# Kernel optimization log

Measured on AMD Instinct MI355X. Metric: run time of the kernel, lower is better.

The kernel has to match this reference:

```python
import jax, jax.numpy as jnp
import numpy as np

H = 1024
V = 50257
S = 8192


def setup_inputs() -> dict:
    key = jax.random.key(0)
    ks = jax.random.split(key, 13)
    s = 0.02  # param init scale
    return {
        "input": jax.random.randint(ks[0], (1,), 0, V),
        "hidden": jax.random.normal(ks[1], (1, 1, H), jnp.float32),
        "encoder_outputs": jax.random.normal(ks[2], (S, H), jnp.float32),
        "embedding": jax.random.normal(ks[3], (V, H), jnp.float32) * s,
        "attn_w": jax.random.normal(ks[4], (1, 2 * H), jnp.float32) * s,
        "attn_b": jnp.zeros((1,), jnp.float32),
        "comb_w": jax.random.normal(ks[5], (H, 2 * H), jnp.float32) * s,
        "comb_b": jnp.zeros((H,), jnp.float32),
        "w_ih": jax.random.normal(ks[6], (3 * H, H), jnp.float32) * s,
        "w_hh": jax.random.normal(ks[7], (3 * H, H), jnp.float32) * s,
        "b_ih": jnp.zeros((3 * H,), jnp.float32),
        "b_hh": jnp.zeros((3 * H,), jnp.float32),
        "out_w": jax.random.normal(ks[8], (V, H), jnp.float32) * s,
        "out_b": jnp.zeros((V,), jnp.float32),
    }


def reference(input, hidden, encoder_outputs, embedding, attn_w, attn_b,
              comb_w, comb_b, w_ih, w_hh, b_ih, b_hh, out_w, out_b):
    # embedded = embedding(input).view(1,1,-1); dropout in eval mode = identity
    emb = embedding[input[0]]            # [H]
    h0 = hidden[0, 0]                    # [H]
    # Original loop computes the SAME score attn(cat(emb, hidden)) for every
    # timestep -> softmax over a constant vector (uniform weights). Compute the
    # scalar once and broadcast (same math, one GEMV instead of S launches).
    score = jnp.concatenate([emb, h0]) @ attn_w[0] + attn_b[0]   # scalar
    seq_len = encoder_outputs.shape[0]
    attn_weights = jax.nn.softmax(jnp.broadcast_to(score, (seq_len,)))  # [S]
    attn_applied = attn_weights @ encoder_outputs                # [H]
    combined = jnp.concatenate([emb, attn_applied]) @ comb_w.T + comb_b  # [H]
    x = jax.nn.relu(combined)
    # Single GRU step (torch nn.GRU gate math)
    gi = w_ih @ x + b_ih                 # [3H]
    gh = w_hh @ h0 + b_hh                # [3H]
    i_r, i_z, i_n = jnp.split(gi, 3)
    h_r, h_z, h_n = jnp.split(gh, 3)
    r = jax.nn.sigmoid(i_r + h_r)
    z = jax.nn.sigmoid(i_z + h_z)
    n = jnp.tanh(i_n + r * h_n)
    h_new = (1.0 - z) * n + z * h0       # [H]
    logits = h_new @ out_w.T + out_b     # [V]
    output = jax.nn.log_softmax(logits)[None, :]   # [1, V]
    return output, h_new[None, None, :], attn_weights[None, :]
```

## Files before the change

kernel.cpp:

```cpp
#include <hip/hip_runtime.h>
#include <math.h>

#define HN 1024
#define VN 50257
#define SN 8192

#define WS_PARTIAL 0
#define WS_AA      262144
#define WS_X       263168
#define WS_GH      264192
#define WS_CEMB    267264
#define WS_HNEW    270336
#define WS_LOGITS  271360
#define WS_EXPD    321618

__device__ __forceinline__ float wred(float v) {
#pragma unroll
  for (int m = 32; m; m >>= 1) v += __shfl_xor(v, m);
  return v;
}

__device__ __forceinline__ float dot4(float4 a, float4 b) {
  return a.x * b.x + a.y * b.y + a.z * b.z + a.w * b.w;
}

__global__ __launch_bounds__(1024) void k1_front(
    const float* __restrict__ enc, const float* __restrict__ w_hh,
    const float* __restrict__ hidden, const int* __restrict__ token,
    const float* __restrict__ embedding, const float* __restrict__ comb_w,
    const float* __restrict__ comb_b, float* __restrict__ ws,
    float* __restrict__ out_attn) {
  const int blk = blockIdx.x, t = threadIdx.x;
  if (blk < 256) {
    __shared__ float4 lds[1024];
    const int g = t >> 8, c4 = t & 255;
    const float4* e4 = (const float4*)enc + ((size_t)blk * 32 + g * 8) * 256 + c4;
    float4 acc = make_float4(0.f, 0.f, 0.f, 0.f);
#pragma unroll
    for (int r = 0; r < 8; ++r) {
      float4 v = e4[r * 256];
      acc.x += v.x; acc.y += v.y; acc.z += v.z; acc.w += v.w;
    }
    lds[t] = acc;
    __syncthreads();
    if (t < 256) {
      float4 a = lds[t], b = lds[t + 256], c = lds[t + 512], d = lds[t + 768];
      float4 s = make_float4(a.x + b.x + c.x + d.x, a.y + b.y + c.y + d.y,
                             a.z + b.z + c.z + d.z, a.w + b.w + c.w + d.w);
      ((float4*)(ws + WS_PARTIAL))[blk * 256 + t] = s;
    }
    if (t < 32) out_attn[blk * 32 + t] = 1.f / 8192.f;
  } else if (blk < 320) {
    const int wg = (blk - 256) * 16 + (t >> 6);
    const int l = t & 63;
    const float4* h4 = (const float4*)hidden;
    float4 hv0 = h4[l], hv1 = h4[64 + l], hv2 = h4[128 + l], hv3 = h4[192 + l];
#pragma unroll
    for (int k = 0; k < 3; ++k) {
      const int r = wg + k * 1024;
      const float4* m4 = (const float4*)w_hh + (size_t)r * 256;
      float acc = dot4(m4[l], hv0) + dot4(m4[64 + l], hv1) +
                  dot4(m4[128 + l], hv2) + dot4(m4[192 + l], hv3);
      acc = wred(acc);
      if (l == 0) ws[WS_GH + r] = acc;
    }
  } else {
    const int i = (blk - 320) * 16 + (t >> 6);
    const int l = t & 63;
    const int tok = token[0];
    const float4* emb4 = (const float4*)embedding + (size_t)tok * 256;
    const float4* cw4 = (const float4*)comb_w + (size_t)i * 512;
    float acc = 0.f;
#pragma unroll
    for (int k = 0; k < 4; ++k) acc += dot4(cw4[k * 64 + l], emb4[k * 64 + l]);
    acc = wred(acc);
    if (l == 0) ws[WS_CEMB + i] = acc + comb_b[i];
  }
}

__global__ void k2_reduce(float* __restrict__ ws) {
  __shared__ float lds[256];
  const int t = threadIdx.x, b = blockIdx.x;
  const int c = b * 32 + (t & 31), rg = t >> 5;
  const float* p = ws + WS_PARTIAL;
  float s = 0.f;
#pragma unroll 8
  for (int j = 0; j < 32; ++j) s += p[(rg * 32 + j) * 1024 + c];
  lds[t] = s;
  __syncthreads();
  if (t < 32) {
    float a = 0.f;
#pragma unroll
    for (int j = 0; j < 8; ++j) a += lds[j * 32 + t];
    ws[WS_AA + b * 32 + t] = a * (1.f / 8192.f);
  }
}

__global__ void k3_x(const float* __restrict__ comb_w, float* __restrict__ ws) {
  const int w = threadIdx.x >> 6, l = threadIdx.x & 63;
  const int i = blockIdx.x * 4 + w;
  const float4* aa4 = (const float4*)(ws + WS_AA);
  const float4* cw4 = (const float4*)comb_w + (size_t)i * 512 + 256;
  float acc = 0.f;
#pragma unroll
  for (int k = 0; k < 4; ++k) acc += dot4(cw4[k * 64 + l], aa4[k * 64 + l]);
  acc = wred(acc);
  if (l == 0) ws[WS_X + i] = fmaxf(ws[WS_CEMB + i] + acc, 0.f);
}

__global__ void k4_gates_h(const float* __restrict__ w_ih,
                           const float* __restrict__ b_ih, const float* __restrict__ b_hh,
                           const float* __restrict__ hidden, float* __restrict__ ws,
                           float* __restrict__ d_out) {
  const int w = threadIdx.x >> 6, l = threadIdx.x & 63;
  const int i = blockIdx.x * 4 + w;
  const float4* x4 = (const float4*)(ws + WS_X);
  float4 xv0 = x4[l], xv1 = x4[64 + l], xv2 = x4[128 + l], xv3 = x4[192 + l];
  const float4* m0 = (const float4*)w_ih + (size_t)i * 256;
  const float4* m1 = (const float4*)w_ih + (size_t)(i + 1024) * 256;
  const float4* m2 = (const float4*)w_ih + (size_t)(i + 2048) * 256;
  float a0 = dot4(m0[l], xv0) + dot4(m0[64 + l], xv1) +
             dot4(m0[128 + l], xv2) + dot4(m0[192 + l], xv3);
  float a1 = dot4(m1[l], xv0) + dot4(m1[64 + l], xv1) +
             dot4(m1[128 + l], xv2) + dot4(m1[192 + l], xv3);
  float a2 = dot4(m2[l], xv0) + dot4(m2[64 + l], xv1) +
             dot4(m2[128 + l], xv2) + dot4(m2[192 + l], xv3);
  a0 = wred(a0); a1 = wred(a1); a2 = wred(a2);
  if (l == 0) {
    float ir = a0 + b_ih[i];
    float iz = a1 + b_ih[i + 1024];
    float inn = a2 + b_ih[i + 2048];
    float hr = ws[WS_GH + i] + b_hh[i];
    float hz = ws[WS_GH + i + 1024] + b_hh[i + 1024];
    float hn = ws[WS_GH + i + 2048] + b_hh[i + 2048];
    float rg = 1.f / (1.f + expf(-(ir + hr)));
    float zg = 1.f / (1.f + expf(-(iz + hz)));
    float ng = tanhf(inn + rg * hn);
    float h = (1.f - zg) * ng + zg * hidden[i];
    ws[WS_HNEW + i] = h;
    d_out[VN + i] = h;
  }
}

__global__ void k5_logits(const float* __restrict__ out_w, const float* __restrict__ out_b,
                          float* __restrict__ ws) {
  const int blk = blockIdx.x, t = threadIdx.x;
  const int w = t >> 6, l = t & 63;
  const int gw = blk * 4 + w;
  __shared__ float4 hs4[256];
  __shared__ double sd[4];
  if (t < 256) hs4[t] = ((const float4*)(ws + WS_HNEW))[t];
  __syncthreads();
  float4 h0_ = hs4[l], h1_ = hs4[64 + l], h2_ = hs4[128 + l], h3_ = hs4[192 + l];
  const float4* ow4 = (const float4*)out_w;
  double eacc = 0.0;
#pragma unroll
  for (int it = 0; it < 2; ++it) {
    const int v0 = gw + it * 24576;
    const float4* r0 = ow4 + (size_t)v0 * 256;
    const float4* r1 = r0 + 8192 * 256;
    const float4* r2 = r1 + 8192 * 256;
    float a0 = dot4(r0[l], h0_) + dot4(r0[64 + l], h1_) +
               dot4(r0[128 + l], h2_) + dot4(r0[192 + l], h3_);
    float a1 = dot4(r1[l], h0_) + dot4(r1[64 + l], h1_) +
               dot4(r1[128 + l], h2_) + dot4(r1[192 + l], h3_);
    float a2 = dot4(r2[l], h0_) + dot4(r2[64 + l], h1_) +
               dot4(r2[128 + l], h2_) + dot4(r2[192 + l], h3_);
    a0 = wred(a0); a1 = wred(a1); a2 = wred(a2);
    if (l == 0) {
      float lg0 = a0 + out_b[v0];
      float lg1 = a1 + out_b[v0 + 8192];
      float lg2 = a2 + out_b[v0 + 16384];
      ws[WS_LOGITS + v0] = lg0;
      ws[WS_LOGITS + v0 + 8192] = lg1;
      ws[WS_LOGITS + v0 + 16384] = lg2;
      eacc += (double)expf(lg0) + (double)expf(lg1) + (double)expf(lg2);
    }
  }
  if (gw < 1105) {
    const int v = gw + 49152;
    const float4* r0 = ow4 + (size_t)v * 256;
    float a = dot4(r0[l], h0_) + dot4(r0[64 + l], h1_) +
              dot4(r0[128 + l], h2_) + dot4(r0[192 + l], h3_);
    a = wred(a);
    if (l == 0) {
      float lg = a + out_b[v];
      ws[WS_LOGITS + v] = lg;
      eacc += (double)expf(lg);
    }
  }
  if (l == 0) sd[w] = eacc;
  __syncthreads();
  if (t == 0) ((double*)(ws + WS_EXPD))[blk] = sd[0] + sd[1] + sd[2] + sd[3];
}

__global__ void k6_final(const float* __restrict__ ws, float* __restrict__ d_out) {
  __shared__ double sd[256];
  const int t = threadIdx.x;
  const double* ed = (const double*)(ws + WS_EXPD);
  double a = 0.0;
#pragma unroll
  for (int j = 0; j < 8; ++j) a += ed[t + j * 256];
  sd[t] = a;
  __syncthreads();
  for (int s = 128; s; s >>= 1) {
    if (t < s) sd[t] += sd[t + s];
    __syncthreads();
  }
  const float logZ = (float)log(sd[0]);
  const int v = blockIdx.x * 256 + t;
  if (v < VN) d_out[v] = ws[WS_LOGITS + v] - logZ;
}

extern "C" void kernel_launch(void* const* d_in, const int* in_sizes, int n_in,
                              void* d_out, int out_size, void* d_ws, size_t ws_size,
                              hipStream_t stream) {
  const int* token = (const int*)d_in[0];
  const float* hidden = (const float*)d_in[1];
  const float* enc = (const float*)d_in[2];
  const float* embedding = (const float*)d_in[3];
  const float* comb_w = (const float*)d_in[6];
  const float* comb_b = (const float*)d_in[7];
  const float* w_ih = (const float*)d_in[8];
  const float* w_hh = (const float*)d_in[9];
  const float* b_ih = (const float*)d_in[10];
  const float* b_hh = (const float*)d_in[11];
  const float* out_w = (const float*)d_in[12];
  const float* out_b = (const float*)d_in[13];
  float* out = (float*)d_out;
  float* ws = (float*)d_ws;

  k1_front<<<384, 1024, 0, stream>>>(enc, w_hh, hidden, token, embedding,
                                     comb_w, comb_b, ws, out + VN + HN);
  k2_reduce<<<32, 256, 0, stream>>>(ws);
  k3_x<<<256, 256, 0, stream>>>(comb_w, ws);
  k4_gates_h<<<256, 256, 0, stream>>>(w_ih, b_ih, b_hh, hidden, ws, out);
  k5_logits<<<2048, 256, 0, stream>>>(out_w, out_b, ws);
  k6_final<<<197, 256, 0, stream>>>(ws, out);
}
```

Baseline: 60.87 us.

## Fuse x and GRU gate kernels via grid barrier, rebalance front and logits work

Merges the combine-projection kernel and the GRU gate kernel into one launch, using a global atomic counter as a grid-wide barrier between the two phases, so one kernel launch and its gap go away. The front kernel's w_hh and comb_w work is redistributed across more blocks, the reduction kernel uses 1024-thread blocks, and the logits kernel uses 2112 blocks processing two rows per iteration with bounds checks instead of a tail branch. The spin barrier relies on all 256 blocks being co-resident, which holds on this GPU but risks deadlock otherwise.

```diff
diff --git a/kernel.cpp b/kernel.cpp
--- a/kernel.cpp
+++ b/kernel.cpp
@@ -13,6 +13,7 @@
 #define WS_HNEW    270336
 #define WS_LOGITS  271360
 #define WS_EXPD    321618
+#define WS_CNT     326100
 
 __device__ __forceinline__ float wred(float v) {
 #pragma unroll
@@ -50,14 +51,14 @@
       ((float4*)(ws + WS_PARTIAL))[blk * 256 + t] = s;
     }
     if (t < 32) out_attn[blk * 32 + t] = 1.f / 8192.f;
-  } else if (blk < 320) {
+  } else if (blk < 352) {
     const int wg = (blk - 256) * 16 + (t >> 6);
     const int l = t & 63;
     const float4* h4 = (const float4*)hidden;
     float4 hv0 = h4[l], hv1 = h4[64 + l], hv2 = h4[128 + l], hv3 = h4[192 + l];
 #pragma unroll
-    for (int k = 0; k < 3; ++k) {
-      const int r = wg + k * 1024;
+    for (int k = 0; k < 2; ++k) {
+      const int r = wg + k * 1536;
       const float4* m4 = (const float4*)w_hh + (size_t)r * 256;
       float acc = dot4(m4[l], hv0) + dot4(m4[64 + l], hv1) +
                   dot4(m4[128 + l], hv2) + dot4(m4[192 + l], hv3);
@@ -65,55 +66,66 @@
       if (l == 0) ws[WS_GH + r] = acc;
     }
   } else {
-    const int i = (blk - 320) * 16 + (t >> 6);
+    const int iw = (blk - 352) * 16 + (t >> 6);
     const int l = t & 63;
     const int tok = token[0];
     const float4* emb4 = (const float4*)embedding + (size_t)tok * 256;
-    const float4* cw4 = (const float4*)comb_w + (size_t)i * 512;
-    float acc = 0.f;
-#pragma unroll
-    for (int k = 0; k < 4; ++k) acc += dot4(cw4[k * 64 + l], emb4[k * 64 + l]);
-    acc = wred(acc);
-    if (l == 0) ws[WS_CEMB + i] = acc + comb_b[i];
-  }
-}
-
-__global__ void k2_reduce(float* __restrict__ ws) {
-  __shared__ float lds[256];
+#pragma unroll
+    for (int k = 0; k < 2; ++k) {
+      const int i = iw + k * 512;
+      const float4* cw4 = (const float4*)comb_w + (size_t)i * 512;
+      float acc = dot4(cw4[l], emb4[l]) + dot4(cw4[64 + l], emb4[64 + l]) +
+                  dot4(cw4[128 + l], emb4[128 + l]) + dot4(cw4[192 + l], emb4[192 + l]);
+      acc = wred(acc);
+      if (l == 0) ws[WS_CEMB + i] = acc + comb_b[i];
+    }
+  }
+}
+
+__global__ __launch_bounds__(1024) void k2_reduce(float* __restrict__ ws) {
+  __shared__ float lds[1024];
   const int t = threadIdx.x, b = blockIdx.x;
+  if (b == 0 && t == 0) ((int*)ws)[WS_CNT] = 0;
   const int c = b * 32 + (t & 31), rg = t >> 5;
   const float* p = ws + WS_PARTIAL;
   float s = 0.f;
-#pragma unroll 8
-  for (int j = 0; j < 32; ++j) s += p[(rg * 32 + j) * 1024 + c];
+#pragma unroll
+  for (int j = 0; j < 8; ++j) s += p[(rg * 8 + j) * 1024 + c];
   lds[t] = s;
   __syncthreads();
   if (t < 32) {
     float a = 0.f;
 #pragma unroll
-    for (int j = 0; j < 8; ++j) a += lds[j * 32 + t];
+    for (int j = 0; j < 32; ++j) a += lds[j * 32 + t];
     ws[WS_AA + b * 32 + t] = a * (1.f / 8192.f);
   }
 }
 
-__global__ void k3_x(const float* __restrict__ comb_w, float* __restrict__ ws) {
+__global__ void k34_x_gates(const float* __restrict__ comb_w,
+                            const float* __restrict__ w_ih,
+                            const float* __restrict__ b_ih, const float* __restrict__ b_hh,
+                            const float* __restrict__ hidden, float* __restrict__ ws,
+                            float* __restrict__ d_out) {
   const int w = threadIdx.x >> 6, l = threadIdx.x & 63;
   const int i = blockIdx.x * 4 + w;
-  const float4* aa4 = (const float4*)(ws + WS_AA);
-  const float4* cw4 = (const float4*)comb_w + (size_t)i * 512 + 256;
-  float acc = 0.f;
-#pragma unroll
-  for (int k = 0; k < 4; ++k) acc += dot4(cw4[k * 64 + l], aa4[k * 64 + l]);
-  acc = wred(acc);
-  if (l == 0) ws[WS_X + i] = fmaxf(ws[WS_CEMB + i] + acc, 0.f);
-}
-
-__global__ void k4_gates_h(const float* __restrict__ w_ih,
-                           const float* __restrict__ b_ih, const float* __restrict__ b_hh,
-                           const float* __restrict__ hidden, float* __restrict__ ws,
-                           float* __restrict__ d_out) {
-  const int w = threadIdx.x >> 6, l = threadIdx.x & 63;
-  const int i = blockIdx.x * 4 + w;
+  {
+    const float4* aa4 = (const float4*)(ws + WS_AA);
+    const float4* cw4 = (const float4*)comb_w + (size_t)i * 512 + 256;
+    float acc = dot4(cw4[l], aa4[l]) + dot4(cw4[64 + l], aa4[64 + l]) +
+                dot4(cw4[128 + l], aa4[128 + l]) + dot4(cw4[192 + l], aa4[192 + l]);
+    acc = wred(acc);
+    if (l == 0) ws[WS_X + i] = fmaxf(ws[WS_CEMB + i] + acc, 0.f);
+  }
+  __threadfence();
+  __syncthreads();
+  int* cnt = (int*)ws + WS_CNT;
+  if (threadIdx.x == 0) {
+    __atomic_fetch_add(cnt, 1, __ATOMIC_ACQ_REL);
+    while (__hip_atomic_load(cnt, __ATOMIC_ACQUIRE, __HIP_MEMORY_SCOPE_AGENT) < 256) {
+    }
+  }
+  __syncthreads();
+  __threadfence();
   const float4* x4 = (const float4*)(ws + WS_X);
   float4 xv0 = x4[l], xv1 = x4[64 + l], xv2 = x4[128 + l], xv3 = x4[192 + l];
   const float4* m0 = (const float4*)w_ih + (size_t)i * 256;
@@ -149,44 +161,33 @@
   const int gw = blk * 4 + w;
   __shared__ float4 hs4[256];
   __shared__ double sd[4];
-  if (t < 256) hs4[t] = ((const float4*)(ws + WS_HNEW))[t];
+  hs4[t] = ((const float4*)(ws + WS_HNEW))[t];
   __syncthreads();
   float4 h0_ = hs4[l], h1_ = hs4[64 + l], h2_ = hs4[128 + l], h3_ = hs4[192 + l];
   const float4* ow4 = (const float4*)out_w;
   double eacc = 0.0;
 #pragma unroll
-  for (int it = 0; it < 2; ++it) {
-    const int v0 = gw + it * 24576;
+  for (int it = 0; it < 3; ++it) {
+    const int v0 = gw + it * 16896;
+    const int v1 = v0 + 8448;
+    const bool ok1 = (v1 < VN);
     const float4* r0 = ow4 + (size_t)v0 * 256;
-    const float4* r1 = r0 + 8192 * 256;
-    const float4* r2 = r1 + 8192 * 256;
+    const float4* r1 = ow4 + (size_t)(ok1 ? v1 : v0) * 256;
     float a0 = dot4(r0[l], h0_) + dot4(r0[64 + l], h1_) +
                dot4(r0[128 + l], h2_) + dot4(r0[192 + l], h3_);
     float a1 = dot4(r1[l], h0_) + dot4(r1[64 + l], h1_) +
                dot4(r1[128 + l], h2_) + dot4(r1[192 + l], h3_);
-    float a2 = dot4(r2[l], h0_) + dot4(r2[64 + l], h1_) +
-               dot4(r2[128 + l], h2_) + dot4(r2[192 + l], h3_);
-    a0 = wred(a0); a1 = wred(a1); a2 = wred(a2);
+    a0 = wred(a0);
+    a1 = wred(a1);
     if (l == 0) {
       float lg0 = a0 + out_b[v0];
-      float lg1 = a1 + out_b[v0 + 8192];
-      float lg2 = a2 + out_b[v0 + 16384];
       ws[WS_LOGITS + v0] = lg0;
-      ws[WS_LOGITS + v0 + 8192] = lg1;
-      ws[WS_LOGITS + v0 + 16384] = lg2;
-      eacc += (double)expf(lg0) + (double)expf(lg1) + (double)expf(lg2);
-    }
-  }
-  if (gw < 1105) {
-    const int v = gw + 49152;
-    const float4* r0 = ow4 + (size_t)v * 256;
-    float a = dot4(r0[l], h0_) + dot4(r0[64 + l], h1_) +
-              dot4(r0[128 + l], h2_) + dot4(r0[192 + l], h3_);
-    a = wred(a);
-    if (l == 0) {
-      float lg = a + out_b[v];
-      ws[WS_LOGITS + v] = lg;
-      eacc += (double)expf(lg);
+      eacc += (double)expf(lg0);
+      if (ok1) {
+        float lg1 = a1 + out_b[v1];
+        ws[WS_LOGITS + v1] = lg1;
+        eacc += (double)expf(lg1);
+      }
     }
   }
   if (l == 0) sd[w] = eacc;
@@ -201,6 +202,7 @@
   double a = 0.0;
 #pragma unroll
   for (int j = 0; j < 8; ++j) a += ed[t + j * 256];
+  if (t < 64) a += ed[t + 2048];
   sd[t] = a;
   __syncthreads();
   for (int s = 128; s; s >>= 1) {
@@ -232,9 +234,8 @@
 
   k1_front<<<384, 1024, 0, stream>>>(enc, w_hh, hidden, token, embedding,
                                      comb_w, comb_b, ws, out + VN + HN);
-  k2_reduce<<<32, 256, 0, stream>>>(ws);
-  k3_x<<<256, 256, 0, stream>>>(comb_w, ws);
-  k4_gates_h<<<256, 256, 0, stream>>>(w_ih, b_ih, b_hh, hidden, ws, out);
-  k5_logits<<<2048, 256, 0, stream>>>(out_w, out_b, ws);
+  k2_reduce<<<32, 1024, 0, stream>>>(ws);
+  k34_x_gates<<<256, 256, 0, stream>>>(comb_w, w_ih, b_ih, b_hh, hidden, ws, out);
+  k5_logits<<<2112, 256, 0, stream>>>(out_w, out_b, ws);
   k6_final<<<197, 256, 0, stream>>>(ws, out);
 }
```

After: 100.1 us. 64.4% more time.
